# Kernel tuning notes

Measured on AMD Instinct MI355X. Metric: run time of the kernel, lower is better.

Reference implementation:

```python
import math
import jax
import jax.numpy as jnp
import numpy as np
from jax import lax

B_, L, D_MODEL = 2, 1024, 2048
D_STATE, D_CONV, EXPAND = 16, 4, 2
D_INNER = EXPAND * D_MODEL          # 4096
DT_RANK = math.ceil(D_MODEL / 16)   # 128


def setup_inputs() -> dict:
    key = jax.random.key(0)
    ks = jax.random.split(key, 8)
    hidden_states = jax.random.normal(ks[0], (B_, L, D_MODEL), jnp.float32)
    in_proj_w = jax.random.normal(ks[1], (2 * D_INNER, D_MODEL), jnp.float32) * (D_MODEL ** -0.5)
    conv_w = jax.random.normal(ks[2], (D_INNER, D_CONV), jnp.float32) * (D_CONV ** -0.5)
    conv_b = jnp.zeros((D_INNER,), jnp.float32)
    x_proj_w = jax.random.normal(ks[3], (DT_RANK + 2 * D_STATE, D_INNER), jnp.float32) * (D_INNER ** -0.5)
    dt_std = DT_RANK ** -0.5
    dt_proj_w = jax.random.uniform(ks[4], (D_INNER, DT_RANK), jnp.float32, minval=-dt_std, maxval=dt_std)
    # dt bias init: softplus^{-1} of dt sampled log-uniform in [1e-3, 1e-1]
    dt = jnp.exp(jax.random.uniform(ks[5], (D_INNER,), jnp.float32)
                 * (math.log(0.1) - math.log(0.001)) + math.log(0.001))
    dt = jnp.clip(dt, 1e-4)
    dt_proj_b = dt + jnp.log(-jnp.expm1(-dt))
    A_log = jnp.log(jnp.broadcast_to(jnp.arange(1, D_STATE + 1, dtype=jnp.float32), (D_INNER, D_STATE)))
    D = jnp.ones((D_INNER,), jnp.float32)
    out_proj_w = jax.random.normal(ks[6], (D_MODEL, D_INNER), jnp.float32) * (D_INNER ** -0.5)
    return {
        'hidden_states': hidden_states, 'in_proj_w': in_proj_w,
        'conv_w': conv_w, 'conv_b': conv_b, 'x_proj_w': x_proj_w,
        'dt_proj_w': dt_proj_w, 'dt_proj_b': dt_proj_b,
        'A_log': A_log, 'D': D, 'out_proj_w': out_proj_w,
    }


def _silu(v):
    return v * jax.nn.sigmoid(v)


def _mamba_forward(hidden_states, in_proj_w, conv_w, conv_b, x_proj_w,
                   dt_proj_w, dt_proj_b, A_log, D, out_proj_w):
    b, l, _ = hidden_states.shape
    # in_proj: (b,l,d_model) -> (b, 2*d_inner, l)
    xz = jnp.einsum('bld,ed->bel', hidden_states, in_proj_w)
    x, z = xz[:, :D_INNER, :], xz[:, D_INNER:, :]
    A = -jnp.exp(A_log.astype(jnp.float32))  # (d_inner, d_state)
    # causal depthwise conv1d + SiLU
    xp = jnp.pad(x, ((0, 0), (0, 0), (D_CONV - 1, 0)))
    x = lax.conv_general_dilated(
        xp, conv_w[:, None, :], window_strides=(1,), padding='VALID',
        dimension_numbers=('NCH', 'OIH', 'NCH'), feature_group_count=D_INNER)
    x = _silu(x + conv_b[None, :, None])  # (b, d_inner, l)
    # x_proj -> dt, B, C
    x_dbl = jnp.einsum('bdl,kd->blk', x, x_proj_w)  # (b,l,dt_rank+2n)
    dt_lo = x_dbl[..., :DT_RANK]
    Bmat = x_dbl[..., DT_RANK:DT_RANK + D_STATE]          # (b,l,n)
    Cmat = x_dbl[..., DT_RANK + D_STATE:]                 # (b,l,n)
    delta = jax.nn.softplus(jnp.einsum('blr,dr->bld', dt_lo, dt_proj_w)
                            + dt_proj_b.astype(jnp.float32))  # (b,l,d)
    xt = jnp.transpose(x, (2, 0, 1))       # (l,b,d)
    dl = jnp.transpose(delta, (1, 0, 2))   # (l,b,d)
    Bl = jnp.transpose(Bmat, (1, 0, 2))    # (l,b,n)
    Cl = jnp.transpose(Cmat, (1, 0, 2))    # (l,b,n)

    def step(h, inp):
        d_t, B_t, C_t, x_t = inp
        dA = jnp.exp(d_t[..., None] * A)                       # (b,d,n)
        h = h * dA + d_t[..., None] * B_t[:, None, :] * x_t[..., None]
        y_t = jnp.sum(h * C_t[:, None, :], axis=-1)            # (b,d)
        return h, y_t

    h0 = jnp.zeros((b, D_INNER, D_STATE), jnp.float32)
    _, ys = lax.scan(step, h0, (dl, Bl, Cl, xt))  # ys: (l,b,d)
    y = jnp.transpose(ys, (1, 0, 2))              # (b,l,d)
    y = y + jnp.transpose(x, (0, 2, 1)) * D[None, None, :]
    y = y * _silu(jnp.transpose(z, (0, 2, 1)))
    out = jnp.einsum('bld,ed->ble', y, out_proj_w)  # (b,l,d_model)
    return out


def reference(hidden_states, in_proj_w, conv_w, conv_b, x_proj_w,
              dt_proj_w, dt_proj_b, A_log, D, out_proj_w):
    return _mamba_forward(hidden_states, in_proj_w, conv_w, conv_b, x_proj_w,
                          dt_proj_w, dt_proj_b, A_log, D, out_proj_w)
```

## Files before the change

### kernel.cpp

```cpp
#include <hip/hip_runtime.h>
#include <hip/hip_bf16.h>
#include <stdint.h>

#define BB 2
#define LL 1024
#define DMODEL 2048
#define DINNER 4096
#define DSTATE 16
#define DTRANK 128
#define XDBL_LD 256
#define CHUNK 64
#define NCH (LL / CHUNK)

typedef unsigned short ushort;
using short8 = __attribute__((ext_vector_type(8))) short;
using f32x4  = __attribute__((ext_vector_type(4))) float;
using us4    = __attribute__((ext_vector_type(4))) ushort;

__device__ __forceinline__ float bf2f(ushort u) {
    union { uint32_t i; float f; } v; v.i = ((uint32_t)u) << 16; return v.f;
}
__device__ __forceinline__ ushort f2bf(float f) {
    union { float f; uint32_t i; } v; v.f = f;
    uint32_t lsb = (v.i >> 16) & 1u;
    uint32_t r = v.i + 0x7FFFu + lsb;
    return (ushort)(r >> 16);
}

__device__ __forceinline__ void glds16(const ushort* g, ushort* l) {
    __builtin_amdgcn_global_load_lds(
        (const __attribute__((address_space(1))) void*)g,
        (__attribute__((address_space(3))) void*)l,
        16, 0, 0);
}

#define BAR()  __builtin_amdgcn_s_barrier()
#define WAITV(n) asm volatile("s_waitcnt vmcnt(" #n ")" ::: "memory")
#define LGKM0() do { asm volatile("s_waitcnt lgkmcnt(0)" ::: "memory"); \
                     __builtin_amdgcn_sched_barrier(0); } while (0)

__global__ __launch_bounds__(256) void cvt_all(
    const float4* __restrict__ hidden, const float4* __restrict__ inproj,
    const float4* __restrict__ dtw, const float4* __restrict__ outp,
    const float4* __restrict__ xproj,
    us4* __restrict__ hid_h, us4* __restrict__ inp_h, us4* __restrict__ dtp_h,
    us4* __restrict__ outp_h, us4* __restrict__ xpp)
{
    long i = (long)blockIdx.x * 256 + threadIdx.x;
    const float4* src; us4* dst; long j;
    if (i < 1048576)      { src = hidden; dst = hid_h;  j = i; }
    else if (i < 5242880) { src = inproj; dst = inp_h;  j = i - 1048576; }
    else if (i < 5373952) { src = dtw;    dst = dtp_h;  j = i - 5242880; }
    else if (i < 7471104) { src = outp;   dst = outp_h; j = i - 5373952; }
    else {
        j = i - 7471104; dst = xpp;
        if (j >= 163840) { us4 z = {0, 0, 0, 0}; dst[j] = z; return; }
        src = xproj;
    }
    float4 v = src[j];
    us4 o; o.x = f2bf(v.x); o.y = f2bf(v.y); o.z = f2bf(v.z); o.w = f2bf(v.w);
    dst[j] = o;
}

template <bool WF, bool WH>
__global__ __launch_bounds__(512, 2) void gemm_nt256(
    const ushort* __restrict__ A, int lda,
    const ushort* __restrict__ Bm, int ldb,
    float* __restrict__ Cf, ushort* __restrict__ Ch, int ldc,
    int K)
{
    __shared__ __align__(16) ushort sA[2][256 * 64];
    __shared__ __align__(16) ushort sB[2][256 * 64];

    const int tid  = threadIdx.x;
    const int lane = tid & 63;
    const int wave = tid >> 6;
    const int wr   = wave >> 2;
    const int wcol = wave & 3;
    const int lrow = lane & 15;
    const int lg   = lane >> 4;
    const int s7   = lane & 7;
    const int kb0 = ((0 + lg) ^ s7) << 4;
    const int kb1 = ((4 + lg) ^ s7) << 4;

    const int NT = gridDim.x, MT = gridDim.y;
    int mt, nt;
    if ((NT & 7) == 0) {
        int lin   = blockIdx.y * NT + blockIdx.x;
        int strip = NT >> 3;
        int xcd   = lin & 7;
        int idx   = lin >> 3;
        nt = xcd * strip + (idx % strip);
        mt = idx / strip;
    } else { mt = blockIdx.y; nt = blockIdx.x; }
    const long m0 = (long)mt * 256;
    const long n0 = (long)nt * 256;

    const long zoff = (long)blockIdx.z;
    A  += zoff * (long)K;
    Bm += zoff * (long)K;
    const long Mrows = (long)MT * 256;
    if (WF) Cf += zoff * Mrows * (long)ldc;

    f32x4 acc[8][4] = {};

    const int sr   = tid >> 3;
    const int scol = (((tid & 7) ^ (sr & 7)) << 3);
    const ushort* Ag = A + (m0 + sr) * (long)lda + scol;
    const int brow_s = ((sr >> 5) << 6) + (sr & 31);
    const ushort* BgS = Bm + (n0 + brow_s) * (long)ldb + scol;

    const int NKT = K >> 6;

    const int arow0 = (wr * 128 + lrow) * 128;
    const int brow0 = (wcol >> 1) * 8192 + (((wcol & 1) << 5) + lrow) * 128;

    auto stageA = [&](int h, ushort* dst, long koff) {
        glds16(Ag + (h * 64) * (long)lda + koff,        dst + h * 4096 + tid * 8);
        glds16(Ag + (h * 64 + 128) * (long)lda + koff,  dst + (h + 2) * 4096 + tid * 8);
    };
    auto stageB = [&](int h, ushort* dst, long koff) {
        glds16(BgS + (32 * h) * (long)ldb + koff,       dst + (2 * h) * 4096 + tid * 8);
        glds16(BgS + (128 + 32 * h) * (long)ldb + koff, dst + (2 * h + 1) * 4096 + tid * 8);
    };

    short8 af[4][2], bf0[2][2], bf1[2][2];

    auto readA = [&](const char* sap, int mh) {
        #pragma unroll
        for (int i4 = 0; i4 < 4; ++i4) {
            const int ab = arow0 + (mh * 64 + i4 * 16) * 128;
            af[i4][0] = *(const short8*)(sap + ab + kb0);
            af[i4][1] = *(const short8*)(sap + ab + kb1);
        }
    };
    auto readB = [&](const char* sbp, int nh, short8 (*bfr)[2]) {
        const int bb = brow0 + nh * 16384;
        #pragma unroll
        for (int j2 = 0; j2 < 2; ++j2) {
            bfr[j2][0] = *(const short8*)(sbp + bb + j2 * (16 * 128) + kb0);
            bfr[j2][1] = *(const short8*)(sbp + bb + j2 * (16 * 128) + kb1);
        }
    };
    auto mfma16 = [&](int mh, int nh, short8 (*bfr)[2]) {
        __builtin_amdgcn_s_setprio(1);
        #pragma unroll
        for (int ks = 0; ks < 2; ++ks)
            #pragma unroll
            for (int i4 = 0; i4 < 4; ++i4)
                #pragma unroll
                for (int j2 = 0; j2 < 2; ++j2)
                    acc[mh * 4 + i4][nh * 2 + j2] =
                        __builtin_amdgcn_mfma_f32_16x16x32_bf16(
                            af[i4][ks], bfr[j2][ks],
                            acc[mh * 4 + i4][nh * 2 + j2], 0, 0, 0);
        __builtin_amdgcn_s_setprio(0);
    };

    stageA(0, &sA[0][0], 0);
    stageB(0, &sB[0][0], 0);
    stageB(1, &sB[0][0], 0);
    stageA(1, &sA[0][0], 0);
    WAITV(4);
    BAR();

    for (int kt = 0; kt < NKT; ++kt) {
        const char* sap = (const char*)&sA[kt & 1][0];
        const char* sbp = (const char*)&sB[kt & 1][0];
        ushort* dA = &sA[(kt & 1) ^ 1][0];
        ushort* dB = &sB[(kt & 1) ^ 1][0];
        const long kn = (long)(kt + 1) << 6;
        const bool pf = (kt + 1 < NKT);

        readA(sap, 0);
        readB(sbp, 0, bf0);
        if (pf) { stageA(0, dA, kn); WAITV(4); } else { WAITV(2); }
        BAR(); LGKM0();
        mfma16(0, 0, bf0);

        readB(sbp, 1, bf1);
        if (pf) { stageB(0, dB, kn); WAITV(4); } else { WAITV(0); }
        BAR(); LGKM0();
        mfma16(0, 1, bf1);

        readA(sap, 1);
        if (pf) stageB(1, dB, kn);
        BAR(); LGKM0();
        mfma16(1, 0, bf0);

        if (pf) { stageA(1, dA, kn); WAITV(4); }
        BAR(); LGKM0();
        mfma16(1, 1, bf1);
    }

    const int r0 = (lane >> 4) * 4;
    const int c0 = lane & 15;
    #pragma unroll
    for (int i = 0; i < 8; ++i) {
        #pragma unroll
        for (int j = 0; j < 4; ++j) {
            const long col = n0 + wcol * 64 + j * 16 + c0;
            #pragma unroll
            for (int r = 0; r < 4; ++r) {
                const long row = m0 + wr * 128 + i * 16 + r0 + r;
                const float v = acc[i][j][r];
                const long idx = row * (long)ldc + col;
                if (WF) Cf[idx] = v;
                if (WH) Ch[idx] = f2bf(v);
            }
        }
    }
}

__global__ __launch_bounds__(512, 2) void gemm_delta(
    const ushort* __restrict__ A,
    const ushort* __restrict__ Bm,
    ushort* __restrict__ Ch,
    const float* __restrict__ bias)
{
    __shared__ __align__(16) ushort sA[128 * 128];
    __shared__ __align__(16) ushort sB[256 * 128];

    const int tid  = threadIdx.x;
    const int lane = tid & 63;
    const int wave = tid >> 6;
    const int wr   = wave >> 2;
    const int wcol = wave & 3;
    const int lrow = lane & 15;
    const int lg   = lane >> 4;
    const int s7r  = lrow & 7;

    const int NT = gridDim.x;
    int mt, nt;
    {
        int lin   = blockIdx.y * NT + blockIdx.x;
        int strip = NT >> 3;
        int xcd   = lin & 7;
        int idx   = lin >> 3;
        nt = xcd * strip + (idx % strip);
        mt = idx / strip;
    }
    const long m0 = (long)mt * 128;
    const long n0 = (long)nt * 256;

    const int srow = tid >> 4;
    const int scol = (((tid & 15) ^ ((tid >> 4) & 7)) << 3);
    const ushort* Ag = A  + (m0 + srow) * (long)XDBL_LD + scol;
    const ushort* Bg = Bm + (n0 + srow) * (long)DTRANK + scol;

    #pragma unroll
    for (int c = 0; c < 4; ++c)
        glds16(Ag + (c * 32) * (long)XDBL_LD, &sA[0] + c * 4096 + tid * 8);
    #pragma unroll
    for (int c = 0; c < 8; ++c)
        glds16(Bg + (c * 32) * (long)DTRANK, &sB[0] + c * 4096 + tid * 8);
    __syncthreads();

    f32x4 acc[4][4] = {};
    const char* sap = (const char*)&sA[0];
    const char* sbp = (const char*)&sB[0];
    const int arow0 = (wr * 64 + lrow) * 256;
    const int brow0 = (wcol * 64 + lrow) * 256;

    #pragma unroll
    for (int ks = 0; ks < 4; ++ks) {
        const int kb = ((ks * 4 + lg) ^ s7r) << 4;
        short8 af[4], bf[4];
        #pragma unroll
        for (int i = 0; i < 4; ++i)
            af[i] = *(const short8*)(sap + arow0 + (i * 16) * 256 + kb);
        #pragma unroll
        for (int j = 0; j < 4; ++j)
            bf[j] = *(const short8*)(sbp + brow0 + (j * 16) * 256 + kb);
        #pragma unroll
        for (int i = 0; i < 4; ++i)
            #pragma unroll
            for (int j = 0; j < 4; ++j)
                acc[i][j] = __builtin_amdgcn_mfma_f32_16x16x32_bf16(
                    af[i], bf[j], acc[i][j], 0, 0, 0);
    }

    const int r0 = (lane >> 4) * 4;
    const int c0 = lane & 15;
    #pragma unroll
    for (int i = 0; i < 4; ++i) {
        #pragma unroll
        for (int j = 0; j < 4; ++j) {
            const long col = n0 + wcol * 64 + j * 16 + c0;
            const float bv = bias[col];
            #pragma unroll
            for (int r = 0; r < 4; ++r) {
                const long row = m0 + wr * 64 + i * 16 + r0 + r;
                float v = acc[i][j][r] + bv;
                v = (v > 20.f) ? v : log1pf(__expf(v));
                Ch[row * (long)DINNER + col] = f2bf(v);
            }
        }
    }
}

template <int EPI, bool WF, bool WH>
__global__ __launch_bounds__(256) void gemm_nt(
    const ushort* __restrict__ A, int lda,
    const ushort* __restrict__ Bm, int ldb,
    float* __restrict__ Cf, ushort* __restrict__ Ch, int ldc,
    int K, const float* __restrict__ bias)
{
    __shared__ __align__(16) ushort sA[128 * 64];
    __shared__ __align__(16) ushort sB[128 * 64];

    const int tid  = threadIdx.x;
    const int lane = tid & 63;
    const int wave = tid >> 6;
    const int wr = wave >> 1, wc = wave & 1;

    const int NT = gridDim.x, MT = gridDim.y;
    int mt, nt;
    if ((NT & 7) == 0) {
        int lin   = blockIdx.y * NT + blockIdx.x;
        int strip = NT >> 3;
        int xcd   = lin & 7;
        int idx   = lin >> 3;
        nt = xcd * strip + (idx % strip);
        mt = idx / strip;
    } else { mt = blockIdx.y; nt = blockIdx.x; }
    const long m0 = (long)mt * 128;
    const long n0 = (long)nt * 128;

    const long zoff = (long)blockIdx.z;
    A  += zoff * (long)K;
    Bm += zoff * (long)K;
    const long Mrows = (long)MT * 128;
    if (WF) Cf += zoff * Mrows * (long)ldc;
    if (WH) Ch += zoff * Mrows * (long)ldc;

    f32x4 acc[4][4] = {};

    const int lrow = lane & 15;
    const int lko  = (lane >> 4) << 3;

    const int sr = tid >> 3;
    const int sc = (tid & 7) << 3;
    const ushort* Ag = A  + (m0 + sr) * (long)lda + sc;
    const ushort* Bg = Bm + (n0 + sr) * (long)ldb + sc;
    ushort* lA = sA + tid * 8;
    ushort* lB = sB + tid * 8;

    for (int k0 = 0; k0 < K; k0 += 64) {
        __syncthreads();
        #pragma unroll
        for (int c = 0; c < 4; ++c) {
            glds16(Ag + (c * 32) * (long)lda + k0, lA + c * 2048);
            glds16(Bg + (c * 32) * (long)ldb + k0, lB + c * 2048);
        }
        __syncthreads();

        #pragma unroll
        for (int ks = 0; ks < 2; ++ks) {
            short8 af[4], bf[4];
            #pragma unroll
            for (int i = 0; i < 4; ++i)
                af[i] = *(const short8*)&sA[(wr * 64 + i * 16 + lrow) * 64 + ks * 32 + lko];
            #pragma unroll
            for (int j = 0; j < 4; ++j)
                bf[j] = *(const short8*)&sB[(wc * 64 + j * 16 + lrow) * 64 + ks * 32 + lko];

            #pragma unroll
            for (int i = 0; i < 4; ++i)
                #pragma unroll
                for (int j = 0; j < 4; ++j)
                    acc[i][j] = __builtin_amdgcn_mfma_f32_16x16x32_bf16(
                        af[i], bf[j], acc[i][j], 0, 0, 0);
        }
    }

    const int r0 = (lane >> 4) * 4;
    const int c0 = lane & 15;
    #pragma unroll
    for (int i = 0; i < 4; ++i) {
        #pragma unroll
        for (int j = 0; j < 4; ++j) {
            long col = n0 + wc * 64 + j * 16 + c0;
            float bv = 0.f;
            if (EPI == 1) bv = bias[col];
            #pragma unroll
            for (int r = 0; r < 4; ++r) {
                long row = m0 + wr * 64 + i * 16 + r0 + r;
                float v = acc[i][j][r];
                if (EPI == 1) {
                    v += bv;
                    v = (v > 20.f) ? v : log1pf(__expf(v));
                }
                long idx = row * (long)ldc + col;
                if (WF) Cf[idx] = v;
                if (WH) Ch[idx] = f2bf(v);
            }
        }
    }
}

template <int NZ, bool WH_>
__global__ __launch_bounds__(256) void reduce_k(
    const float4* __restrict__ parts, long stride4, int n4,
    float4* __restrict__ outF, us4* __restrict__ outH)
{
    int i = blockIdx.x * 256 + threadIdx.x;
    if (i >= n4) return;
    float4 s = parts[i];
    #pragma unroll
    for (int z = 1; z < NZ; ++z) {
        float4 v = parts[(long)z * stride4 + i];
        s.x += v.x; s.y += v.y; s.z += v.z; s.w += v.w;
    }
    if (outF) outF[i] = s;
    if (WH_) {
        us4 o; o.x = f2bf(s.x); o.y = f2bf(s.y); o.z = f2bf(s.z); o.w = f2bf(s.w);
        outH[i] = o;
    }
}

__global__ __launch_bounds__(256) void conv_silu_kernel(
    const ushort* __restrict__ xz,
    const float* __restrict__ cw,
    const float* __restrict__ cb,
    ushort* __restrict__ xc)
{
    int gid = blockIdx.x * 256 + threadIdx.x;
    int d  = gid & (DINNER - 1);
    int rl = gid >> 12;
    int l  = rl & (LL - 1);
    float acc = cb[d];
    #pragma unroll
    for (int j = 0; j < 4; ++j) {
        int li = l - 3 + j;
        if (li >= 0)
            acc += cw[d * 4 + j] * bf2f(xz[(long)(rl - 3 + j) * 8192 + d]);
    }
    float s = acc / (1.f + __expf(-acc));
    xc[gid] = f2bf(s);
}

__global__ __launch_bounds__(256) void scan_p1(
    const ushort* __restrict__ delta,
    const ushort* __restrict__ xc,
    const float*  __restrict__ xdbl,
    const float*  __restrict__ A_log,
    float* __restrict__ Hbuf,
    float* __restrict__ sumdt_buf)
{
    __shared__ float sB[CHUNK * 16];
    const int tid = threadIdx.x;
    const int k = blockIdx.y, b = blockIdx.z;
    const int d = blockIdx.x * 256 + tid;
    const int row0 = b * LL + k * CHUNK;

    #pragma unroll
    for (int i = 0; i < 4; ++i) {
        int idx = i * 256 + tid;
        sB[idx] = xdbl[(long)(row0 + (idx >> 4)) * XDBL_LD + DTRANK + (idx & 15)];
    }
    __syncthreads();

    float A[DSTATE];
    const float4* Ap = (const float4*)(A_log + d * DSTATE);
    #pragma unroll
    for (int i = 0; i < 4; ++i) {
        float4 v = Ap[i];
        A[i*4+0] = -__expf(v.x); A[i*4+1] = -__expf(v.y);
        A[i*4+2] = -__expf(v.z); A[i*4+3] = -__expf(v.w);
    }

    float H[DSTATE];
    #pragma unroll
    for (int s = 0; s < DSTATE; ++s) H[s] = 0.f;
    float sumdt = 0.f;

    for (int t = 0; t < CHUNK; ++t) {
        const long row = row0 + t;
        const float dt = bf2f(delta[row * DINNER + d]);
        const float xv = bf2f(xc[row * DINNER + d]);
        const float dx = dt * xv;
        sumdt += dt;
        #pragma unroll
        for (int s = 0; s < DSTATE; ++s) {
            float dA = __expf(dt * A[s]);
            H[s] = H[s] * dA + dx * sB[t * 16 + s];
        }
    }

    const long o = ((long)(b * NCH + k) * DINNER + d) * DSTATE;
    float4* Ho = (float4*)(Hbuf + o);
    #pragma unroll
    for (int i = 0; i < 4; ++i) {
        float4 v; v.x = H[i*4+0]; v.y = H[i*4+1]; v.z = H[i*4+2]; v.w = H[i*4+3];
        Ho[i] = v;
    }
    sumdt_buf[(b * NCH + k) * DINNER + d] = sumdt;
}

__global__ __launch_bounds__(256) void scan_p2(
    const float* __restrict__ A_log,
    const float* __restrict__ sumdt_buf,
    float* __restrict__ Hbuf)
{
    int gid = blockIdx.x * 256 + threadIdx.x;
    int b = gid >> 16;
    int rem = gid & 65535;
    int d = rem >> 4, s = rem & 15;
    float A = -__expf(A_log[d * DSTATE + s]);
    float h = 0.f;
    for (int k = 0; k < NCH; ++k) {
        long idx = ((long)(b * NCH + k) * DINNER + d) * DSTATE + s;
        float Hk = Hbuf[idx];
        float sd = sumdt_buf[(b * NCH + k) * DINNER + d];
        Hbuf[idx] = h;
        h = h * __expf(A * sd) + Hk;
    }
}

__global__ __launch_bounds__(256) void scan_p3(
    const ushort* __restrict__ delta,
    const ushort* __restrict__ xc,
    const float*  __restrict__ xdbl,
    const ushort* __restrict__ xz,
    const float*  __restrict__ A_log,
    const float*  __restrict__ Dp,
    const float*  __restrict__ hin,
    ushort* __restrict__ y)
{
    __shared__ float sBC[CHUNK * 32];
    const int tid = threadIdx.x;
    const int k = blockIdx.y, b = blockIdx.z;
    const int d = blockIdx.x * 256 + tid;
    const int row0 = b * LL + k * CHUNK;

    #pragma unroll
    for (int i = 0; i < 8; ++i) {
        int idx = i * 256 + tid;
        sBC[idx] = xdbl[(long)(row0 + (idx >> 5)) * XDBL_LD + DTRANK + (idx & 31)];
    }
    __syncthreads();

    float A[DSTATE];
    const float4* Ap = (const float4*)(A_log + d * DSTATE);
    #pragma unroll
    for (int i = 0; i < 4; ++i) {
        float4 v = Ap[i];
        A[i*4+0] = -__expf(v.x); A[i*4+1] = -__expf(v.y);
        A[i*4+2] = -__expf(v.z); A[i*4+3] = -__expf(v.w);
    }
    const float Dd = Dp[d];

    float h[DSTATE];
    const float4* Hp = (const float4*)(hin + ((long)(b * NCH + k) * DINNER + d) * DSTATE);
    #pragma unroll
    for (int i = 0; i < 4; ++i) {
        float4 v = Hp[i];
        h[i*4+0] = v.x; h[i*4+1] = v.y; h[i*4+2] = v.z; h[i*4+3] = v.w;
    }

    for (int t = 0; t < CHUNK; ++t) {
        const long row = row0 + t;
        const float dt = bf2f(delta[row * DINNER + d]);
        const float xv = bf2f(xc[row * DINNER + d]);
        const float dx = dt * xv;
        float yt = 0.f;
        #pragma unroll
        for (int s = 0; s < DSTATE; ++s) {
            float dA = __expf(dt * A[s]);
            h[s] = h[s] * dA + dx * sBC[t * 32 + s];
            yt += h[s] * sBC[t * 32 + 16 + s];
        }
        yt += xv * Dd;
        const float zv = bf2f(xz[row * 8192 + DINNER + d]);
        yt *= zv / (1.f + __expf(-zv));
        y[row * DINNER + d] = f2bf(yt);
    }
}

extern "C" void kernel_launch(void* const* d_in, const int* in_sizes, int n_in,
                              void* d_out, int out_size, void* d_ws, size_t ws_size,
                              hipStream_t stream)
{
    const float* hidden    = (const float*)d_in[0];
    const float* in_proj   = (const float*)d_in[1];
    const float* conv_w    = (const float*)d_in[2];
    const float* conv_b    = (const float*)d_in[3];
    const float* x_proj    = (const float*)d_in[4];
    const float* dt_proj_w = (const float*)d_in[5];
    const float* dt_proj_b = (const float*)d_in[6];
    const float* A_log     = (const float*)d_in[7];
    const float* Dp        = (const float*)d_in[8];
    const float* out_proj  = (const float*)d_in[9];
    float* out = (float*)d_out;

    char* ws = (char*)d_ws;
    ushort* xz_h    = (ushort*)(ws);
    ushort* xc      = (ushort*)(ws + 33554432);
    ushort* xpp     = (ushort*)(ws + 50331648);
    float*  xdbl    = (float*)(ws + 52428800);
    ushort* xdblh   = (ushort*)(ws + 54525952);
    ushort* delta_h = (ushort*)(ws + 55574528);
    ushort* yb      = (ushort*)(ws + 72351744);
    ushort* hid_h   = (ushort*)(ws + 89128960);
    ushort* inp_h   = (ushort*)(ws + 97517568);
    float*  parts   = (float*)(ws + 97517568);
    float*  Hbuf    = (float*)(ws + 97517568);
    float*  sumdt   = (float*)(ws + 105906176);
    ushort* dtp_h   = (ushort*)(ws + 131072000);
    ushort* outp_h  = (ushort*)(ws + 132120576);
    float*  parts2  = (float*)(ws);

    const int M = BB * LL;

    cvt_all<<<30208, 256, 0, stream>>>(
        (const float4*)hidden, (const float4*)in_proj, (const float4*)dt_proj_w,
        (const float4*)out_proj, (const float4*)x_proj,
        (us4*)hid_h, (us4*)inp_h, (us4*)dtp_h, (us4*)outp_h, (us4*)xpp);

    gemm_nt256<false, true><<<dim3(8192 / 256, M / 256), 512, 0, stream>>>(
        hid_h, DMODEL, inp_h, DMODEL, nullptr, xz_h, 8192, DMODEL);

    conv_silu_kernel<<<(M * DINNER) / 256, 256, 0, stream>>>(xz_h, conv_w, conv_b, xc);

    gemm_nt<0, true, false><<<dim3(XDBL_LD / 128, M / 128, 16), 256, 0, stream>>>(
        xc, DINNER, xpp, DINNER, parts, nullptr, XDBL_LD, DINNER / 16, nullptr);
    reduce_k<16, true><<<(M * XDBL_LD / 4 + 255) / 256, 256, 0, stream>>>(
        (const float4*)parts, (long)M * XDBL_LD / 4, M * XDBL_LD / 4,
        (float4*)xdbl, (us4*)xdblh);

    gemm_delta<<<dim3(DINNER / 256, M / 128), 512, 0, stream>>>(
        xdblh, dtp_h, delta_h, dt_proj_b);

    scan_p1<<<dim3(DINNER / 256, NCH, BB), 256, 0, stream>>>(
        delta_h, xc, xdbl, A_log, Hbuf, sumdt);
    scan_p2<<<(BB * DINNER * DSTATE) / 256, 256, 0, stream>>>(
        A_log, sumdt, Hbuf);
    scan_p3<<<dim3(DINNER / 256, NCH, BB), 256, 0, stream>>>(
        delta_h, xc, xdbl, xz_h, A_log, Dp, Hbuf, yb);

    gemm_nt256<true, false><<<dim3(DMODEL / 256, M / 256, 4), 512, 0, stream>>>(
        yb, DINNER, outp_h, DINNER, parts2, nullptr, DMODEL, DINNER / 4);
    reduce_k<4, false><<<(M * DMODEL / 4 + 255) / 256, 256, 0, stream>>>(
        (const float4*)parts2, (long)M * DMODEL / 4, M * DMODEL / 4,
        (float4*)out, nullptr);
}
```

Before: 453.7 us.

## Replace split-K out_proj GEMM with 128x128 direct-write GEMM; grid-stride conversion kernel

The out_proj GEMM previously used 256x256 tiles with 4-way split-K, writing fp32 partials and then running a separate reduction kernel. It now uses a new 128x128-tile, 256-thread double-buffered MFMA kernel with XCD-aware tile remapping. This kernel runs the full K and writes the output directly, which removes the partial-buffer traffic and the reduce launch. The cost is less reuse per tile and a longer K loop per block, giving 256 blocks. The conversion kernel also switches to a grid-stride loop over 2048 blocks instead of launching about 30k blocks.

```diff
diff --git a/kernel.cpp b/kernel.cpp
--- a/kernel.cpp
+++ b/kernel.cpp
@@ -39,6 +39,7 @@
 #define LGKM0() do { asm volatile("s_waitcnt lgkmcnt(0)" ::: "memory"); \
                      __builtin_amdgcn_sched_barrier(0); } while (0)
 
+#define CVT_TOTAL 7733248L
 __global__ __launch_bounds__(256) void cvt_all(
     const float4* __restrict__ hidden, const float4* __restrict__ inproj,
     const float4* __restrict__ dtw, const float4* __restrict__ outp,
@@ -46,20 +47,22 @@
     us4* __restrict__ hid_h, us4* __restrict__ inp_h, us4* __restrict__ dtp_h,
     us4* __restrict__ outp_h, us4* __restrict__ xpp)
 {
-    long i = (long)blockIdx.x * 256 + threadIdx.x;
-    const float4* src; us4* dst; long j;
-    if (i < 1048576)      { src = hidden; dst = hid_h;  j = i; }
-    else if (i < 5242880) { src = inproj; dst = inp_h;  j = i - 1048576; }
-    else if (i < 5373952) { src = dtw;    dst = dtp_h;  j = i - 5242880; }
-    else if (i < 7471104) { src = outp;   dst = outp_h; j = i - 5373952; }
-    else {
-        j = i - 7471104; dst = xpp;
-        if (j >= 163840) { us4 z = {0, 0, 0, 0}; dst[j] = z; return; }
-        src = xproj;
-    }
-    float4 v = src[j];
-    us4 o; o.x = f2bf(v.x); o.y = f2bf(v.y); o.z = f2bf(v.z); o.w = f2bf(v.w);
-    dst[j] = o;
+    for (long i = (long)blockIdx.x * 256 + threadIdx.x; i < CVT_TOTAL;
+         i += (long)gridDim.x * 256) {
+        const float4* src; us4* dst; long j;
+        if (i < 1048576)      { src = hidden; dst = hid_h;  j = i; }
+        else if (i < 5242880) { src = inproj; dst = inp_h;  j = i - 1048576; }
+        else if (i < 5373952) { src = dtw;    dst = dtp_h;  j = i - 5242880; }
+        else if (i < 7471104) { src = outp;   dst = outp_h; j = i - 5373952; }
+        else {
+            j = i - 7471104; dst = xpp;
+            if (j >= 163840) { us4 z = {0, 0, 0, 0}; dst[j] = z; continue; }
+            src = xproj;
+        }
+        float4 v = src[j];
+        us4 o; o.x = f2bf(v.x); o.y = f2bf(v.y); o.z = f2bf(v.z); o.w = f2bf(v.w);
+        dst[j] = o;
+    }
 }
 
 template <bool WF, bool WH>
@@ -203,6 +206,127 @@
             #pragma unroll
             for (int r = 0; r < 4; ++r) {
                 const long row = m0 + wr * 128 + i * 16 + r0 + r;
+                const float v = acc[i][j][r];
+                const long idx = row * (long)ldc + col;
+                if (WF) Cf[idx] = v;
+                if (WH) Ch[idx] = f2bf(v);
+            }
+        }
+    }
+}
+
+template <bool WF, bool WH>
+__global__ __launch_bounds__(256, 2) void gemm_nt128d(
+    const ushort* __restrict__ A, int lda,
+    const ushort* __restrict__ Bm, int ldb,
+    float* __restrict__ Cf, ushort* __restrict__ Ch, int ldc,
+    int K)
+{
+    __shared__ __align__(16) ushort sA[2][128 * 64];
+    __shared__ __align__(16) ushort sB[2][128 * 64];
+
+    const int tid  = threadIdx.x;
+    const int lane = tid & 63;
+    const int wave = tid >> 6;
+    const int wr   = wave >> 1;
+    const int wc   = wave & 1;
+    const int lrow = lane & 15;
+    const int lg   = lane >> 4;
+    const int s7   = lane & 7;
+    const int kb0 = ((0 + lg) ^ s7) << 4;
+    const int kb1 = ((4 + lg) ^ s7) << 4;
+
+    const int NT = gridDim.x, MT = gridDim.y;
+    int mt, nt;
+    if ((NT & 7) == 0) {
+        int lin   = blockIdx.y * NT + blockIdx.x;
+        int strip = NT >> 3;
+        int xcd   = lin & 7;
+        int idx   = lin >> 3;
+        nt = xcd * strip + (idx % strip);
+        mt = idx / strip;
+    } else { mt = blockIdx.y; nt = blockIdx.x; }
+    const long m0 = (long)mt * 128;
+    const long n0 = (long)nt * 128;
+
+    f32x4 acc[4][4] = {};
+
+    const int sr   = tid >> 3;
+    const int scol = (((tid & 7) ^ (sr & 7)) << 3);
+    const ushort* Ag = A  + (m0 + sr) * (long)lda + scol;
+    const ushort* Bg = Bm + (n0 + sr) * (long)ldb + scol;
+
+    const int NKT = K >> 6;
+
+    {
+        ushort* dA0 = &sA[0][0] + tid * 8;
+        ushort* dB0 = &sB[0][0] + tid * 8;
+        #pragma unroll
+        for (int c = 0; c < 4; ++c) {
+            glds16(Ag + (c * 32) * (long)lda, dA0 + c * 2048);
+            glds16(Bg + (c * 32) * (long)ldb, dB0 + c * 2048);
+        }
+    }
+    __syncthreads();
+
+    const int arow0 = (wr * 64 + lrow) * 128;
+    const int brow0 = (wc * 64 + lrow) * 128;
+
+    for (int kt = 0; kt < NKT; ++kt) {
+        const int p = kt & 1;
+        const char* sap = (const char*)&sA[p][0];
+        const char* sbp = (const char*)&sB[p][0];
+        ushort* dA = &sA[p ^ 1][0] + tid * 8;
+        ushort* dB = &sB[p ^ 1][0] + tid * 8;
+        const long kn = (long)(kt + 1) << 6;
+        const bool pf = (kt + 1 < NKT);
+
+        short8 af[4][2], bf[4][2];
+        #pragma unroll
+        for (int i = 0; i < 4; ++i) {
+            const int ab = arow0 + (i * 16) * 128;
+            af[i][0] = *(const short8*)(sap + ab + kb0);
+            af[i][1] = *(const short8*)(sap + ab + kb1);
+        }
+        #pragma unroll
+        for (int j = 0; j < 4; ++j) {
+            const int bb = brow0 + (j * 16) * 128;
+            bf[j][0] = *(const short8*)(sbp + bb + kb0);
+            bf[j][1] = *(const short8*)(sbp + bb + kb1);
+        }
+
+        if (pf) {
+            #pragma unroll
+            for (int c = 0; c < 4; ++c) {
+                glds16(Ag + (c * 32) * (long)lda + kn, dA + c * 2048);
+                glds16(Bg + (c * 32) * (long)ldb + kn, dB + c * 2048);
+            }
+        }
+
+        __builtin_amdgcn_s_setprio(1);
+        #pragma unroll
+        for (int ks = 0; ks < 2; ++ks)
+            #pragma unroll
+            for (int i = 0; i < 4; ++i)
+                #pragma unroll
+                for (int j = 0; j < 4; ++j)
+                    acc[i][j] = __builtin_amdgcn_mfma_f32_16x16x32_bf16(
+                        af[i][ks], bf[j][ks], acc[i][j], 0, 0, 0);
+        __builtin_amdgcn_s_setprio(0);
+
+        __syncthreads();
+    }
+
+    const int r0 = (lane >> 4) * 4;
+    const int c0 = lane & 15;
+    #pragma unroll
+    for (int i = 0; i < 4; ++i) {
+        #pragma unroll
+        for (int j = 0; j < 4; ++j) {
+            const long col = n0 + wc * 64 + j * 16 + c0;
+            #pragma unroll
+            for (int r = 0; r < 4; ++r) {
+                const long row = m0 + wr * 64 + i * 16 + r0 + r;
                 const float v = acc[i][j][r];
                 const long idx = row * (long)ldc + col;
                 if (WF) Cf[idx] = v;
@@ -609,11 +733,10 @@
     float*  sumdt   = (float*)(ws + 105906176);
     ushort* dtp_h   = (ushort*)(ws + 131072000);
     ushort* outp_h  = (ushort*)(ws + 132120576);
-    float*  parts2  = (float*)(ws);
 
     const int M = BB * LL;
 
-    cvt_all<<<30208, 256, 0, stream>>>(
+    cvt_all<<<2048, 256, 0, stream>>>(
         (const float4*)hidden, (const float4*)in_proj, (const float4*)dt_proj_w,
         (const float4*)out_proj, (const float4*)x_proj,
         (us4*)hid_h, (us4*)inp_h, (us4*)dtp_h, (us4*)outp_h, (us4*)xpp);
@@ -639,9 +762,6 @@
     scan_p3<<<dim3(DINNER / 256, NCH, BB), 256, 0, stream>>>(
         delta_h, xc, xdbl, xz_h, A_log, Dp, Hbuf, yb);
 
-    gemm_nt256<true, false><<<dim3(DMODEL / 256, M / 256, 4), 512, 0, stream>>>(
-        yb, DINNER, outp_h, DINNER, parts2, nullptr, DMODEL, DINNER / 4);
-    reduce_k<4, false><<<(M * DMODEL / 4 + 255) / 256, 256, 0, stream>>>(
-        (const float4*)parts2, (long)M * DMODEL / 4, M * DMODEL / 4,
-        (float4*)out, nullptr);
-}
+    gemm_nt128d<true, false><<<dim3(DMODEL / 128, M / 128), 256, 0, stream>>>(
+        yb, DINNER, outp_h, DINNER, out, nullptr, DMODEL, DINNER);
+}
```

After: 496.7 us. 9.5% more time.
